# Optimization experiments

Hardware: AMD Instinct MI355X
Metric: run time of the kernel (lower is better)

The kernel has to match this reference:

```python
import jax, jax.numpy as jnp
import numpy as np
from jax import lax

B, T, D, H, L, V = 4, 512, 768, 768, 2, 50257


def setup_inputs() -> dict:
    key = jax.random.key(0)
    ks = jax.random.split(key, 4)
    std = 0.02
    return {
        "reps": jax.random.normal(ks[0], (B, T, D), dtype=jnp.float32),
        "W_ih": jax.random.normal(ks[1], (L, 4 * H, D), dtype=jnp.float32) * std,
        "W_hh": jax.random.normal(ks[2], (L, 4 * H, H), dtype=jnp.float32) * std,
        "b": jnp.zeros((L, 4 * H), dtype=jnp.float32),
        "head_w": jax.random.normal(ks[3], (V, H), dtype=jnp.float32) * std,
        "head_b": jnp.zeros((V,), dtype=jnp.float32),
    }


def _lstm_layer(x_tbd, W_i, W_h, bias):
    # x_tbd: (T, B, in); returns (T, B, H) hidden sequence
    b_sz = x_tbd.shape[1]
    h_dim = W_h.shape[1]
    # precompute input projections for all timesteps: (T, B, 4H)
    xg = jnp.einsum('tbd,gd->tbg', x_tbd, W_i) + bias

    def step(carry, xt_g):
        h, c = carry
        gates = xt_g + h @ W_h.T  # (B, 4H)
        i, f, g, o = jnp.split(gates, 4, axis=-1)
        i = jax.nn.sigmoid(i)
        f = jax.nn.sigmoid(f)
        g = jnp.tanh(g)
        o = jax.nn.sigmoid(o)
        c2 = f * c + i * g
        h2 = o * jnp.tanh(c2)
        return (h2, c2), h2

    h0 = jnp.zeros((b_sz, h_dim), dtype=x_tbd.dtype)
    c0 = jnp.zeros((b_sz, h_dim), dtype=x_tbd.dtype)
    _, ys = lax.scan(step, (h0, c0), xg)
    return ys


def reference(reps, W_ih, W_hh, b, head_w, head_b):
    # reps: (B, T, D) -> logits (B, T, V)
    x = jnp.swapaxes(reps, 0, 1)  # (T, B, D)
    n_layers = W_ih.shape[0]
    for l in range(n_layers):
        x = _lstm_layer(x, W_ih[l], W_hh[l], b[l])
    hidden = jnp.swapaxes(x, 0, 1)  # (B, T, H)
    return jnp.einsum('bth,vh->btv', hidden, head_w) + head_b
```

## Files before the change

kernel.cpp:

```cpp
#include <hip/hip_runtime.h>
#include <hip/hip_fp16.h>
#include <cstdint>

#define B_SZ 4
#define T_SZ 512
#define D_SZ 768
#define H_SZ 768
#define G4   3072
#define V_SZ 50257
#define V_PAD 50304
#define M_SZ 2048
#define FUSE_WGS 192

using half8 = __attribute__((ext_vector_type(8))) _Float16;
using f32x4 = __attribute__((ext_vector_type(4))) float;
typedef unsigned long long ull;


__global__ void conv_A0(const float* __restrict__ reps, _Float16* __restrict__ A0) {
  int idx = blockIdx.x * blockDim.x + threadIdx.x;
  const int total = M_SZ * D_SZ;
  for (; idx < total; idx += gridDim.x * blockDim.x) {
    int k = idx % D_SZ, m = idx / D_SZ;
    int t = m >> 2, b = m & 3;
    A0[idx] = (_Float16)reps[(b * T_SZ + t) * D_SZ + k];
  }
}

__global__ void conv_cast(const float* __restrict__ src, _Float16* __restrict__ dst, int n) {
  int idx = blockIdx.x * blockDim.x + threadIdx.x;
  for (; idx < n; idx += gridDim.x * blockDim.x) dst[idx] = (_Float16)src[idx];
}

__global__ void conv_head(const float* __restrict__ w, _Float16* __restrict__ dst) {
  int idx = blockIdx.x * blockDim.x + threadIdx.x;
  const int total = V_PAD * H_SZ;
  for (; idx < total; idx += gridDim.x * blockDim.x) {
    int n = idx / H_SZ, k = idx % H_SZ;
    dst[idx] = (n < V_SZ) ? (_Float16)w[n * H_SZ + k] : (_Float16)0.f;
  }
}


__global__ __launch_bounds__(256) void gemm_bt_f16(
    const _Float16* __restrict__ A, const _Float16* __restrict__ B,
    const float* __restrict__ bias, float* __restrict__ C,
    int M, int N, int K, int mode, int Nreal)
{
  __shared__ __align__(16) _Float16 As[128][32];
  __shared__ __align__(16) _Float16 Bs[128][32];
  const int t = threadIdx.x;
  const int lane = t & 63, w = t >> 6;
  const int wr = w >> 1, wc = w & 1;
  const int m0 = blockIdx.x * 128, n0 = blockIdx.y * 128;

  f32x4 acc[4][4] = {};

  const int srow = t >> 2;
  const int scol = (t & 3) * 8;

  const _Float16* ga0 = &A[(size_t)(m0 + srow) * K + scol];
  const _Float16* ga1 = &A[(size_t)(m0 + 64 + srow) * K + scol];
  const _Float16* gb0 = &B[(size_t)(n0 + srow) * K + scol];
  const _Float16* gb1 = &B[(size_t)(n0 + 64 + srow) * K + scol];
  _Float16* lA0 = &As[0][0] + w * 512;
  _Float16* lA1 = &As[64][0] + w * 512;
  _Float16* lB0 = &Bs[0][0] + w * 512;
  _Float16* lB1 = &Bs[64][0] + w * 512;

  for (int k0 = 0; k0 < K; k0 += 32) {
    __syncthreads();
    __builtin_amdgcn_global_load_lds(ga0 + k0, lA0, 16, 0, 0);
    __builtin_amdgcn_global_load_lds(ga1 + k0, lA1, 16, 0, 0);
    __builtin_amdgcn_global_load_lds(gb0 + k0, lB0, 16, 0, 0);
    __builtin_amdgcn_global_load_lds(gb1 + k0, lB1, 16, 0, 0);
    asm volatile("s_waitcnt vmcnt(0)" ::: "memory");
    __syncthreads();

    const int fr = lane & 15, k8 = (lane >> 4) * 8;
    half8 af[4], bf[4];
#pragma unroll
    for (int i = 0; i < 4; ++i) {
      af[i] = *(const half8*)&As[wr * 64 + i * 16 + fr][k8];
      bf[i] = *(const half8*)&Bs[wc * 64 + i * 16 + fr][k8];
    }
#pragma unroll
    for (int i = 0; i < 4; ++i)
#pragma unroll
      for (int j = 0; j < 4; ++j)
        acc[i][j] = __builtin_amdgcn_mfma_f32_16x16x32_f16(af[i], bf[j], acc[i][j], 0, 0, 0);
  }

  const int fr = lane & 15, rq = lane >> 4;
#pragma unroll
  for (int i = 0; i < 4; ++i) {
#pragma unroll
    for (int j = 0; j < 4; ++j) {
      int n = n0 + wc * 64 + j * 16 + fr;
      if (n >= Nreal) continue;
      float bv = bias[n];
#pragma unroll
      for (int r = 0; r < 4; ++r) {
        int m = m0 + wr * 64 + i * 16 + rq * 4 + r;
        float v = acc[i][j][r] + bv;
        if (mode == 0) {
          C[(size_t)m * N + n] = v;
        } else {
          int tt = m >> 2, bb = m & 3;
          C[(size_t)(bb * T_SZ + tt) * V_SZ + n] = v;
        }
      }
    }
  }
}


__global__ __launch_bounds__(256) void lstm_fused(
    const float* __restrict__ xg0,
    const float* __restrict__ Wih1,
    const float* __restrict__ Whh,
    const float* __restrict__ bias,
    ull* __restrict__ hx0p,
    ull* __restrict__ hx1p,
    _Float16* __restrict__ h1hist)
{
  __shared__ __align__(16) float h0buf[G4];
  __shared__ __align__(16) float h1buf[G4];
  __shared__ __align__(16) float red[4][8][4][4];
  __shared__ float actv[4][8][4];
  __shared__ float cst[8][4];

  const int t = threadIdx.x, lane = t & 63, wv = t >> 6;
  const bool L1 = blockIdx.x >= 96;
  const int lid = L1 ? (blockIdx.x - 96) : blockIdx.x;
  const int j0 = lid * 8;

  const float* WhhL = Whh + (L1 ? (size_t)G4 * H_SZ : 0);

  float wreg[8][12];
#pragma unroll
  for (int c = 0; c < 8; ++c)
#pragma unroll
    for (int kk = 0; kk < 12; ++kk)
      wreg[c][kk] = WhhL[(size_t)(wv * H_SZ + j0 + c) * H_SZ + kk * 64 + lane];

  float wreg2[8][12];
  if (L1) {
#pragma unroll
    for (int c = 0; c < 8; ++c)
#pragma unroll
      for (int kk = 0; kk < 12; ++kk)
        wreg2[c][kk] = Wih1[(size_t)(wv * H_SZ + j0 + c) * H_SZ + kk * 64 + lane];
  }

  const int g_ = t >> 5, c_ = (t >> 2) & 7, b_ = t & 3;

  float breg = 0.f;
  if (L1 && t < 128) breg = bias[G4 + g_ * H_SZ + j0 + c_];

  if (t < 32) cst[t >> 2][t & 3] = 0.f;

  const int elim = L1 ? 513 : 512;
  for (int e = 0; e < elim; ++e) {
    if (L1 && e == 0) {
      if (t < 32) {
        int c = t >> 2, b = t & 3;
        __hip_atomic_store(&hx1p[(size_t)(j0 + c) * 4 + b], (ull)1u << 32,
                           __ATOMIC_RELAXED, __HIP_MEMORY_SCOPE_AGENT);
      }
      continue;
    }

    float xgv = 0.f;
    if (!L1 && t < 128)
      xgv = xg0[(size_t)((e << 2) + b_) * G4 + g_ * H_SZ + j0 + c_];

    if (!L1 && t == 0 && e >= 5) {
      const ull* bp = hx1p + (size_t)((e - 5) & 7) * G4;
      while ((unsigned)(__hip_atomic_load(bp, __ATOMIC_RELAXED, __HIP_MEMORY_SCOPE_AGENT) >> 32)
             < (unsigned)(e - 4))
        __builtin_amdgcn_s_sleep(1);
    }

    const unsigned need = (unsigned)e;

    {
      const ull* s0 = hx0p + (size_t)((e + 7) & 7) * G4;
      ull v[12];
#pragma unroll
      for (int i = 0; i < 12; ++i)
        v[i] = __hip_atomic_load(&s0[t + i * 256], __ATOMIC_RELAXED, __HIP_MEMORY_SCOPE_AGENT);
      for (;;) {
        bool stale = false;
#pragma unroll
        for (int i = 0; i < 12; ++i) stale |= ((unsigned)(v[i] >> 32) < need);
        if (!stale) break;
        __builtin_amdgcn_s_sleep(1);
#pragma unroll
        for (int i = 0; i < 12; ++i)
          if ((unsigned)(v[i] >> 32) < need)
            v[i] = __hip_atomic_load(&s0[t + i * 256], __ATOMIC_RELAXED, __HIP_MEMORY_SCOPE_AGENT);
      }
#pragma unroll
      for (int i = 0; i < 12; ++i) h0buf[t + i * 256] = __uint_as_float((unsigned)v[i]);
    }
    if (L1) {
      const ull* s1 = hx1p + (size_t)((e + 7) & 7) * G4;
      ull v[12];
#pragma unroll
      for (int i = 0; i < 12; ++i)
        v[i] = __hip_atomic_load(&s1[t + i * 256], __ATOMIC_RELAXED, __HIP_MEMORY_SCOPE_AGENT);
      for (;;) {
        bool stale = false;
#pragma unroll
        for (int i = 0; i < 12; ++i) stale |= ((unsigned)(v[i] >> 32) < need);
        if (!stale) break;
        __builtin_amdgcn_s_sleep(1);
#pragma unroll
        for (int i = 0; i < 12; ++i)
          if ((unsigned)(v[i] >> 32) < need)
            v[i] = __hip_atomic_load(&s1[t + i * 256], __ATOMIC_RELAXED, __HIP_MEMORY_SCOPE_AGENT);
      }
#pragma unroll
      for (int i = 0; i < 12; ++i) h1buf[t + i * 256] = __uint_as_float((unsigned)v[i]);
    }
    __syncthreads();

    float4 acc[8];
#pragma unroll
    for (int c = 0; c < 8; ++c) acc[c] = make_float4(0.f, 0.f, 0.f, 0.f);

    if (!L1) {
#pragma unroll
      for (int kk = 0; kk < 12; ++kk) {
        float4 h4 = *(const float4*)&h0buf[(kk * 64 + lane) * 4];
#pragma unroll
        for (int c = 0; c < 8; ++c) {
          float wf = wreg[c][kk];
          acc[c].x = fmaf(wf, h4.x, acc[c].x);
          acc[c].y = fmaf(wf, h4.y, acc[c].y);
          acc[c].z = fmaf(wf, h4.z, acc[c].z);
          acc[c].w = fmaf(wf, h4.w, acc[c].w);
        }
      }
    } else {
#pragma unroll
      for (int kk = 0; kk < 12; ++kk) {
        float4 x4 = *(const float4*)&h0buf[(kk * 64 + lane) * 4];
        float4 h4 = *(const float4*)&h1buf[(kk * 64 + lane) * 4];
#pragma unroll
        for (int c = 0; c < 8; ++c) {
          float wx = wreg2[c][kk], wh = wreg[c][kk];
          acc[c].x = fmaf(wx, x4.x, fmaf(wh, h4.x, acc[c].x));
          acc[c].y = fmaf(wx, x4.y, fmaf(wh, h4.y, acc[c].y));
          acc[c].z = fmaf(wx, x4.z, fmaf(wh, h4.z, acc[c].z));
          acc[c].w = fmaf(wx, x4.w, fmaf(wh, h4.w, acc[c].w));
        }
      }
    }

#pragma unroll
    for (int mask = 1; mask <= 8; mask <<= 1) {
#pragma unroll
      for (int c = 0; c < 8; ++c) {
        acc[c].x += __shfl_xor(acc[c].x, mask, 64);
        acc[c].y += __shfl_xor(acc[c].y, mask, 64);
        acc[c].z += __shfl_xor(acc[c].z, mask, 64);
        acc[c].w += __shfl_xor(acc[c].w, mask, 64);
      }
    }
    if ((lane & 15) == 0) {
      int q = lane >> 4;
#pragma unroll
      for (int c = 0; c < 8; ++c) *(float4*)&red[wv][c][q][0] = acc[c];
    }
    __syncthreads();

    if (t < 128) {
      float s = red[g_][c_][0][b_] + red[g_][c_][1][b_] + red[g_][c_][2][b_] + red[g_][c_][3][b_]
              + (L1 ? breg : xgv);
      actv[g_][c_][b_] = (g_ == 2) ? tanhf(s) : (1.f / (1.f + expf(-s)));
    }
    __syncthreads();

    if (t < 32) {
      int c = t >> 2, b = t & 3;
      float iv = actv[0][c][b], fv = actv[1][c][b], gv = actv[2][c][b], ov = actv[3][c][b];
      float cn = fv * cst[c][b] + iv * gv;
      cst[c][b] = cn;
      float hn = ov * tanhf(cn);
      ull p = ((ull)(unsigned)(e + 1) << 32) | (ull)__float_as_uint(hn);
      ull* dst = (L1 ? hx1p : hx0p) + (size_t)(e & 7) * G4;
      __hip_atomic_store(&dst[(size_t)(j0 + c) * 4 + b], p,
                         __ATOMIC_RELAXED, __HIP_MEMORY_SCOPE_AGENT);
      if (L1)
        h1hist[(size_t)(((e - 1) << 2) + b) * H_SZ + j0 + c] = (_Float16)hn;
    }
  }
}


extern "C" void kernel_launch(void* const* d_in, const int* in_sizes, int n_in,
                              void* d_out, int out_size, void* d_ws, size_t ws_size,
                              hipStream_t stream) {
  const float* reps   = (const float*)d_in[0];
  const float* W_ih   = (const float*)d_in[1];
  const float* W_hh   = (const float*)d_in[2];
  const float* bias   = (const float*)d_in[3];
  const float* head_w = (const float*)d_in[4];
  const float* head_b = (const float*)d_in[5];
  float* out = (float*)d_out;

  char* ws = (char*)d_ws;
  _Float16* A0h    = (_Float16*)(ws + 0);
  _Float16* Wih_h  = (_Float16*)(ws + 3145728);
  _Float16* Whead  = (_Float16*)(ws + 12582912);
  float*    xg0    = (float*)   (ws + 89849856);
  _Float16* h1hist = (_Float16*)(ws + 115015680);
  ull*      hx0p   = (ull*)     (ws + 118161408);
  ull*      hx1p   = (ull*)     (ws + 118358016);

  hipLaunchKernelGGL(conv_A0,   dim3(1024), dim3(256), 0, stream, reps, A0h);
  hipLaunchKernelGGL(conv_cast, dim3(1024), dim3(256), 0, stream, W_ih, Wih_h, G4 * D_SZ);
  hipLaunchKernelGGL(conv_head, dim3(4096), dim3(256), 0, stream, head_w, Whead);

  hipLaunchKernelGGL(gemm_bt_f16, dim3(16, 24), dim3(256), 0, stream,
                     A0h, Wih_h, bias, xg0, M_SZ, G4, H_SZ, 0, G4);

  hipMemsetAsync(hx0p, 0, 393216, stream);
  hipLaunchKernelGGL(lstm_fused, dim3(FUSE_WGS), dim3(256), 0, stream,
                     xg0, W_ih + (size_t)G4 * D_SZ, W_hh, bias,
                     hx0p, hx1p, h1hist);

  hipLaunchKernelGGL(gemm_bt_f16, dim3(16, 393), dim3(256), 0, stream,
                     h1hist, Whead, head_b, out, M_SZ, V_PAD, H_SZ, 1, V_SZ);
}
```

Measured before the change: 3.009 ms.

## Pack hidden-state exchange as fp16 pairs and fuse gate activation into one stage

```diff
diff --git a/kernel.cpp b/kernel.cpp
--- a/kernel.cpp
+++ b/kernel.cpp
@@ -11,10 +11,18 @@
 #define V_PAD 50304
 #define M_SZ 2048
 #define FUSE_WGS 192
+#define RWORDS 1536
 
 using half8 = __attribute__((ext_vector_type(8))) _Float16;
 using f32x4 = __attribute__((ext_vector_type(4))) float;
 typedef unsigned long long ull;
+
+static __device__ __forceinline__ unsigned short f16bits(_Float16 x) {
+  union { _Float16 f; unsigned short u; } cv; cv.f = x; return cv.u;
+}
+static __device__ __forceinline__ float f16val(unsigned short u) {
+  union { unsigned short u; _Float16 f; } cv; cv.u = u; return (float)cv.f;
+}
 
 
 __global__ void conv_A0(const float* __restrict__ reps, _Float16* __restrict__ A0) {
@@ -127,8 +135,6 @@
   __shared__ __align__(16) float h0buf[G4];
   __shared__ __align__(16) float h1buf[G4];
   __shared__ __align__(16) float red[4][8][4][4];
-  __shared__ float actv[4][8][4];
-  __shared__ float cst[8][4];
 
   const int t = threadIdx.x, lane = t & 63, wv = t >> 6;
   const bool L1 = blockIdx.x >= 96;
@@ -153,76 +159,91 @@
         wreg2[c][kk] = Wih1[(size_t)(wv * H_SZ + j0 + c) * H_SZ + kk * 64 + lane];
   }
 
-  const int g_ = t >> 5, c_ = (t >> 2) & 7, b_ = t & 3;
-
-  float breg = 0.f;
-  if (L1 && t < 128) breg = bias[G4 + g_ * H_SZ + j0 + c_];
-
-  if (t < 32) cst[t >> 2][t & 3] = 0.f;
+  const int cc = t >> 2, cb = t & 3;
+  float cstate = 0.f;
+  float breg4[4] = {0.f, 0.f, 0.f, 0.f};
+  if (L1 && t < 32) {
+#pragma unroll
+    for (int g = 0; g < 4; ++g) breg4[g] = bias[G4 + g * H_SZ + j0 + cc];
+  }
 
   const int elim = L1 ? 513 : 512;
   for (int e = 0; e < elim; ++e) {
     if (L1 && e == 0) {
-      if (t < 32) {
-        int c = t >> 2, b = t & 3;
-        __hip_atomic_store(&hx1p[(size_t)(j0 + c) * 4 + b], (ull)1u << 32,
+      if (t < 16)
+        __hip_atomic_store(&hx1p[(size_t)(j0 * 2 + t)], (ull)1u << 32,
                            __ATOMIC_RELAXED, __HIP_MEMORY_SCOPE_AGENT);
-      }
       continue;
     }
 
-    float xgv = 0.f;
-    if (!L1 && t < 128)
-      xgv = xg0[(size_t)((e << 2) + b_) * G4 + g_ * H_SZ + j0 + c_];
+    float xg4[4] = {0.f, 0.f, 0.f, 0.f};
+    if (!L1 && t < 32) {
+      const float* xp = xg0 + (size_t)((e << 2) + cb) * G4 + j0 + cc;
+#pragma unroll
+      for (int g = 0; g < 4; ++g) xg4[g] = xp[g * H_SZ];
+    }
 
     if (!L1 && t == 0 && e >= 5) {
-      const ull* bp = hx1p + (size_t)((e - 5) & 7) * G4;
+      const ull* bp = hx1p + (size_t)((e - 5) & 7) * RWORDS;
       while ((unsigned)(__hip_atomic_load(bp, __ATOMIC_RELAXED, __HIP_MEMORY_SCOPE_AGENT) >> 32)
              < (unsigned)(e - 4))
         __builtin_amdgcn_s_sleep(1);
     }
 
     const unsigned need = (unsigned)e;
-
+    const size_t slot = (size_t)((e + 7) & 7) * RWORDS;
+
+    ull v0[6], v1[6];
     {
-      const ull* s0 = hx0p + (size_t)((e + 7) & 7) * G4;
-      ull v[12];
-#pragma unroll
-      for (int i = 0; i < 12; ++i)
-        v[i] = __hip_atomic_load(&s0[t + i * 256], __ATOMIC_RELAXED, __HIP_MEMORY_SCOPE_AGENT);
+      const ull* s0 = hx0p + slot;
+      const ull* s1 = hx1p + slot;
+#pragma unroll
+      for (int i = 0; i < 6; ++i)
+        v0[i] = __hip_atomic_load(&s0[t + i * 256], __ATOMIC_RELAXED, __HIP_MEMORY_SCOPE_AGENT);
+      if (L1) {
+#pragma unroll
+        for (int i = 0; i < 6; ++i)
+          v1[i] = __hip_atomic_load(&s1[t + i * 256], __ATOMIC_RELAXED, __HIP_MEMORY_SCOPE_AGENT);
+      }
       for (;;) {
         bool stale = false;
 #pragma unroll
-        for (int i = 0; i < 12; ++i) stale |= ((unsigned)(v[i] >> 32) < need);
+        for (int i = 0; i < 6; ++i) stale |= ((unsigned)(v0[i] >> 32) < need);
+        if (L1) {
+#pragma unroll
+          for (int i = 0; i < 6; ++i) stale |= ((unsigned)(v1[i] >> 32) < need);
+        }
         if (!stale) break;
         __builtin_amdgcn_s_sleep(1);
 #pragma unroll
-        for (int i = 0; i < 12; ++i)
-          if ((unsigned)(v[i] >> 32) < need)
-            v[i] = __hip_atomic_load(&s0[t + i * 256], __ATOMIC_RELAXED, __HIP_MEMORY_SCOPE_AGENT);
-      }
-#pragma unroll
-      for (int i = 0; i < 12; ++i) h0buf[t + i * 256] = __uint_as_float((unsigned)v[i]);
-    }
-    if (L1) {
-      const ull* s1 = hx1p + (size_t)((e + 7) & 7) * G4;
-      ull v[12];
-#pragma unroll
-      for (int i = 0; i < 12; ++i)
-        v[i] = __hip_atomic_load(&s1[t + i * 256], __ATOMIC_RELAXED, __HIP_MEMORY_SCOPE_AGENT);
-      for (;;) {
-        bool stale = false;
-#pragma unroll
-        for (int i = 0; i < 12; ++i) stale |= ((unsigned)(v[i] >> 32) < need);
-        if (!stale) break;
-        __builtin_amdgcn_s_sleep(1);
-#pragma unroll
-        for (int i = 0; i < 12; ++i)
-          if ((unsigned)(v[i] >> 32) < need)
-            v[i] = __hip_atomic_load(&s1[t + i * 256], __ATOMIC_RELAXED, __HIP_MEMORY_SCOPE_AGENT);
-      }
-#pragma unroll
-      for (int i = 0; i < 12; ++i) h1buf[t + i * 256] = __uint_as_float((unsigned)v[i]);
+        for (int i = 0; i < 6; ++i)
+          if ((unsigned)(v0[i] >> 32) < need)
+            v0[i] = __hip_atomic_load(&s0[t + i * 256], __ATOMIC_RELAXED, __HIP_MEMORY_SCOPE_AGENT);
+        if (L1) {
+#pragma unroll
+          for (int i = 0; i < 6; ++i)
+            if ((unsigned)(v1[i] >> 32) < need)
+              v1[i] = __hip_atomic_load(&s1[t + i * 256], __ATOMIC_RELAXED, __HIP_MEMORY_SCOPE_AGENT);
+        }
+      }
+#pragma unroll
+      for (int i = 0; i < 6; ++i) {
+        int w2 = (t + i * 256) * 2;
+        unsigned pl = (unsigned)v0[i];
+        float2 f; f.x = f16val((unsigned short)(pl & 0xffff));
+        f.y = f16val((unsigned short)(pl >> 16));
+        *(float2*)&h0buf[w2] = f;
+      }
+      if (L1) {
+#pragma unroll
+        for (int i = 0; i < 6; ++i) {
+          int w2 = (t + i * 256) * 2;
+          unsigned pl = (unsigned)v1[i];
+          float2 f; f.x = f16val((unsigned short)(pl & 0xffff));
+          f.y = f16val((unsigned short)(pl >> 16));
+          *(float2*)&h1buf[w2] = f;
+        }
+      }
     }
     __syncthreads();
 
@@ -276,25 +297,29 @@
     }
     __syncthreads();
 
-    if (t < 128) {
-      float s = red[g_][c_][0][b_] + red[g_][c_][1][b_] + red[g_][c_][2][b_] + red[g_][c_][3][b_]
-              + (L1 ? breg : xgv);
-      actv[g_][c_][b_] = (g_ == 2) ? tanhf(s) : (1.f / (1.f + expf(-s)));
-    }
-    __syncthreads();
-
     if (t < 32) {
-      int c = t >> 2, b = t & 3;
-      float iv = actv[0][c][b], fv = actv[1][c][b], gv = actv[2][c][b], ov = actv[3][c][b];
-      float cn = fv * cst[c][b] + iv * gv;
-      cst[c][b] = cn;
-      float hn = ov * tanhf(cn);
-      ull p = ((ull)(unsigned)(e + 1) << 32) | (ull)__float_as_uint(hn);
-      ull* dst = (L1 ? hx1p : hx0p) + (size_t)(e & 7) * G4;
-      __hip_atomic_store(&dst[(size_t)(j0 + c) * 4 + b], p,
-                         __ATOMIC_RELAXED, __HIP_MEMORY_SCOPE_AGENT);
+      float s[4];
+#pragma unroll
+      for (int g = 0; g < 4; ++g)
+        s[g] = red[g][cc][0][cb] + red[g][cc][1][cb] + red[g][cc][2][cb] + red[g][cc][3][cb]
+             + (L1 ? breg4[g] : xg4[g]);
+      float iv = 1.f / (1.f + expf(-s[0]));
+      float fv = 1.f / (1.f + expf(-s[1]));
+      float gv = tanhf(s[2]);
+      float ov = 1.f / (1.f + expf(-s[3]));
+      cstate = fv * cstate + iv * gv;
+      float hn = ov * tanhf(cstate);
+      float hp = __shfl_xor(hn, 1, 64);
+      if ((cb & 1) == 0) {
+        unsigned pl = (unsigned)f16bits((_Float16)hn)
+                    | ((unsigned)f16bits((_Float16)hp) << 16);
+        ull p = ((ull)(unsigned)(e + 1) << 32) | (ull)pl;
+        ull* dst = (L1 ? hx1p : hx0p) + (size_t)(e & 7) * RWORDS;
+        __hip_atomic_store(&dst[(j0 + cc) * 2 + (cb >> 1)], p,
+                           __ATOMIC_RELAXED, __HIP_MEMORY_SCOPE_AGENT);
+      }
       if (L1)
-        h1hist[(size_t)(((e - 1) << 2) + b) * H_SZ + j0 + c] = (_Float16)hn;
+        h1hist[(size_t)(((e - 1) << 2) + cb) * H_SZ + j0 + cc] = (_Float16)hn;
     }
   }
 }
@@ -318,7 +343,7 @@
   float*    xg0    = (float*)   (ws + 89849856);
   _Float16* h1hist = (_Float16*)(ws + 115015680);
   ull*      hx0p   = (ull*)     (ws + 118161408);
-  ull*      hx1p   = (ull*)     (ws + 118358016);
+  ull*      hx1p   = (ull*)     (ws + 118259712);
 
   hipLaunchKernelGGL(conv_A0,   dim3(1024), dim3(256), 0, stream, reps, A0h);
   hipLaunchKernelGGL(conv_cast, dim3(1024), dim3(256), 0, stream, W_ih, Wih_h, G4 * D_SZ);
@@ -327,7 +352,7 @@
   hipLaunchKernelGGL(gemm_bt_f16, dim3(16, 24), dim3(256), 0, stream,
                      A0h, Wih_h, bias, xg0, M_SZ, G4, H_SZ, 0, G4);
 
-  hipMemsetAsync(hx0p, 0, 393216, stream);
+  hipMemsetAsync(hx0p, 0, 196608, stream);
   hipLaunchKernelGGL(lstm_fused, dim3(FUSE_WGS), dim3(256), 0, stream,
                      xg0, W_ih + (size_t)G4 * D_SZ, W_hh, bias,
                      hx0p, hx1p, h1hist);
```

New measurement: 3.541 ms. 17.7% more time.
